# Kernel optimization log

Hardware: AMD Instinct MI355X
Metric: run time of the kernel (lower is better)

## Reference

```python
import jax, jax.numpy as jnp
import numpy as np
from jax import lax

B, S, I, H, O, L = 32, 512, 256, 1024, 256, 3


def setup_inputs() -> dict:
    key = jax.random.key(0)
    ks = jax.random.split(key, 10)
    sc = 0.02
    return {
        "x": jax.random.normal(ks[0], (B, S, I), dtype=jnp.float32),
        "h0": jnp.zeros((B, L, H), dtype=jnp.float32),
        # layer 0 params: gates ordered [z, r, g]
        "Wx0": jax.random.normal(ks[1], (3, H, I), dtype=jnp.float32) * sc,
        "Wh0": jax.random.normal(ks[2], (3, H, H), dtype=jnp.float32) * sc,
        "bh0": jax.random.normal(ks[3], (3, H), dtype=jnp.float32) * sc,
        # layers 1..L-1 params (input dim = H)
        "Wx": jax.random.normal(ks[4], (L - 1, 3, H, H), dtype=jnp.float32) * sc,
        "Wh": jax.random.normal(ks[5], (L - 1, 3, H, H), dtype=jnp.float32) * sc,
        "bh": jax.random.normal(ks[6], (L - 1, 3, H), dtype=jnp.float32) * sc,
        "Wout": jax.random.normal(ks[7], (O, H), dtype=jnp.float32) * sc,
        "bout": jax.random.normal(ks[8], (O,), dtype=jnp.float32) * sc,
    }


def _gru_layer(x_seq, h0, Wx, Wh, bh):
    # x_seq: [S,B,Iin], h0: [B,H], Wx: [3,H,Iin], Wh: [3,H,H], bh: [3,H]
    # Precompute all input projections once (fused GEMM over full sequence).
    xproj = jnp.einsum('sbi,ghi->sbgh', x_seq, Wx)  # [S,B,3,H]

    def step(h, xp):
        z = jax.nn.sigmoid(xp[:, 0] + h @ Wh[0].T + bh[0])
        r = jax.nn.sigmoid(xp[:, 1] + h @ Wh[1].T + bh[1])
        g = jnp.tanh(xp[:, 2] + (r * h) @ Wh[2].T + bh[2])
        h_new = z * h + (1.0 - z) * g
        return h_new, h_new

    h_last, hs = lax.scan(step, h0, xproj)
    return hs, h_last  # hs: [S,B,H]


def reference(x, h0, Wx0, Wh0, bh0, Wx, Wh, bh, Wout, bout):
    seq = jnp.transpose(x, (1, 0, 2))  # [S,B,I]
    cur, hl = _gru_layer(seq, h0[:, 0], Wx0, Wh0, bh0)
    finals = [hl]
    n_extra = Wx.shape[0]
    for i in range(n_extra):  # small fixed layer count
        cur, hl = _gru_layer(cur, h0[:, i + 1], Wx[i], Wh[i], bh[i])
        finals.append(hl)
    out = cur @ Wout.T + bout  # [S,B,O]
    layer_output = jnp.transpose(out, (1, 0, 2))  # [B,S,O]
    hidden_state = jnp.stack(finals, axis=1)  # [B,L,H]
    return layer_output, hidden_state
```

## Files before the change

### kernel.cpp

```cpp
#include <hip/hip_runtime.h>
#include <cstdint>
#include <cstddef>

#define S_  512
#define H_  1024
#define H3  3072
#define OUT_OFF 4194304

typedef __attribute__((ext_vector_type(8))) short  short8;
typedef __attribute__((ext_vector_type(4))) float  f32x4;
typedef __attribute__((ext_vector_type(4))) unsigned short us4;
typedef __attribute__((ext_vector_type(4))) unsigned int   u32x4;
typedef unsigned long long u64;

#define MFMA __builtin_amdgcn_mfma_f32_16x16x32_bf16

static const size_t XP_OFF    = 0;
static const size_t H2_OFF    = 100663296;
static const size_t XBF_OFF   = 134217728;
static const size_t WX0B_OFF  = 142606336;
static const size_t WZR0_OFF  = 144179200;
static const size_t WG0_OFF   = 148373504;
static const size_t WZR1_OFF  = 150470656;
static const size_t WGX1_OFF  = 158859264;
static const size_t WG1_OFF   = 160956416;
static const size_t WZR2_OFF  = 163053568;
static const size_t WGX2_OFF  = 171442176;
static const size_t WG2_OFF   = 173539328;
static const size_t WOUTB_OFF = 175636480;
static const size_t ZBU_OFF   = 176160768;
static const size_t GXB_OFF   = 176553984;
static const size_t HROW_OFF  = 176947200;
static const size_t FLAG_OFF  = 177340416;
static const size_t HH_OFF    = 177344512;
static const size_t RHH_OFF   = 278597632;
static const size_t WS_HIST   = 379654144;
static const size_t WS_BASE   = 177737728;

__device__ inline unsigned short f2bf(float f){
  unsigned u = __builtin_bit_cast(unsigned, f);
  unsigned r = u + 0x7fffu + ((u >> 16) & 1u);
  return (unsigned short)(r >> 16);
}
__device__ inline float bf2f(unsigned short s){
  unsigned u = ((unsigned)s) << 16;
  return __builtin_bit_cast(float, u);
}
__device__ inline unsigned ld_sys(const unsigned* p){
  return __hip_atomic_load(p, __ATOMIC_RELAXED, __HIP_MEMORY_SCOPE_AGENT);
}
__device__ inline void st_sys(unsigned* p, unsigned v){
  __hip_atomic_store(p, v, __ATOMIC_RELAXED, __HIP_MEMORY_SCOPE_AGENT);
}
__device__ inline u64 ld64(const u64* p){
  return __hip_atomic_load(p, __ATOMIC_RELAXED, __HIP_MEMORY_SCOPE_AGENT);
}
__device__ inline void st64(u64* p, u64 v){
  __hip_atomic_store(p, v, __ATOMIC_RELAXED, __HIP_MEMORY_SCOPE_AGENT);
}
template<bool HIST>
__device__ inline u64 LD(const u64* p){
  if constexpr (HIST) return *p; else return ld64(p);
}
__device__ inline short8 mk8u(u64 a, u64 b){
  u32x4 u; u.x = (unsigned)a; u.y = (unsigned)(a >> 32); u.z = (unsigned)b; u.w = (unsigned)(b >> 32);
  return __builtin_bit_cast(short8, u);
}
__device__ inline u64 pk4(float a, float b, float c, float d){
  return (u64)f2bf(a) | ((u64)f2bf(b) << 16) | ((u64)f2bf(c) << 32) | ((u64)f2bf(d) << 48);
}
__device__ inline u64 pk2f(float a, float b){
  return (u64)__builtin_bit_cast(unsigned, a) | ((u64)__builtin_bit_cast(unsigned, b) << 32);
}
__device__ inline float lo32f(u64 u){ return __builtin_bit_cast(float, (unsigned)u); }
__device__ inline float hi32f(u64 u){ return __builtin_bit_cast(float, (unsigned)(u >> 32)); }

__global__ void k_conv(const float* __restrict__ src, unsigned short* __restrict__ dst, int n){
  int i = blockIdx.x*256 + threadIdx.x;
  if (i < n) dst[i] = f2bf(src[i]);
}
__global__ void k_packzr(const float* __restrict__ Wh, const float* __restrict__ Wx,
                         unsigned short* __restrict__ dst){
  size_t i = (size_t)blockIdx.x*256 + threadIdx.x;
  int k = (int)(i & 2047);
  int n = (int)(i >> 11);
  float v = (k < 1024) ? Wh[(size_t)n*1024 + k] : Wx[(size_t)n*1024 + (k - 1024)];
  dst[i] = f2bf(v);
}
__global__ void k_convx(const float* __restrict__ x, unsigned short* __restrict__ xbf){
  int row = blockIdx.x;
  int s = row >> 5, b = row & 31;
  int i = threadIdx.x;
  xbf[(size_t)row*256 + i] = f2bf(x[((size_t)b*S_ + s)*256 + i]);
}

__global__ __launch_bounds__(256) void k_gemm(const unsigned short* __restrict__ A,
                                              const unsigned short* __restrict__ Bw,
                                              const float* __restrict__ bias,
                                              void* __restrict__ Cout,
                                              int Kd, int mode, int Nd){
  __shared__ __align__(16) unsigned short lA[128*40];
  __shared__ __align__(16) unsigned short lB[128*40];
  int bm = blockIdx.y * 128, bn = blockIdx.x * 128;
  int tid = threadIdx.x;
  int w = tid >> 6, lane = tid & 63, q = lane >> 4, cc = lane & 15;
  int wm = (w >> 1) * 64, wn = (w & 1) * 64;
  f32x4 acc[4][4] = {};
  for (int k0 = 0; k0 < Kd; k0 += 32){
    #pragma unroll
    for (int i = 0; i < 2; i++){
      int idx = tid + i*256;
      int r = idx >> 2, ch = idx & 3;
      int m = bm + r;
      int arow = (mode == 0) ? m : ((m & 511)*32 + (m >> 9));
      *(u32x4*)(lA + r*40 + ch*8) = *(const u32x4*)(A + (size_t)arow*Kd + k0 + ch*8);
      *(u32x4*)(lB + r*40 + ch*8) = *(const u32x4*)(Bw + (size_t)(bn + r)*Kd + k0 + ch*8);
    }
    __syncthreads();
    short8 af[4], bfv[4];
    #pragma unroll
    for (int i = 0; i < 4; i++) af[i]  = *(const short8*)(lA + (wm + i*16 + cc)*40 + q*8);
    #pragma unroll
    for (int i = 0; i < 4; i++) bfv[i] = *(const short8*)(lB + (wn + i*16 + cc)*40 + q*8);
    #pragma unroll
    for (int i = 0; i < 4; i++)
      #pragma unroll
      for (int j = 0; j < 4; j++)
        acc[i][j] = MFMA(af[i], bfv[j], acc[i][j], 0, 0, 0);
    __syncthreads();
  }
  if (mode == 0){
    unsigned short* xp = (unsigned short*)Cout;
    #pragma unroll
    for (int i = 0; i < 4; i++){
      #pragma unroll
      for (int j = 0; j < 4; j++){
        int m = bm + wm + i*16 + q*4;
        int n = bn + wn + j*16 + cc;
        float bv = bias[n];
        int s = m >> 5, b0 = m & 31;
        us4 pk;
        #pragma unroll
        for (int reg = 0; reg < 4; reg++) pk[reg] = f2bf(acc[i][j][reg] + bv);
        *(us4*)(xp + ((size_t)s*H3 + n)*32 + b0) = pk;
      }
    }
  } else {
    float* C = (float*)Cout;
    #pragma unroll
    for (int i = 0; i < 4; i++){
      #pragma unroll
      for (int j = 0; j < 4; j++){
        int m = bm + wm + i*16 + q*4;
        int n = bn + wn + j*16 + cc;
        float bv = bias[n];
        #pragma unroll
        for (int reg = 0; reg < 4; reg++)
          C[(size_t)(m + reg)*Nd + n] = acc[i][j][reg] + bv;
      }
    }
  }
}

__device__ inline void gbar(unsigned* flags, unsigned ep){
  __syncthreads();
  if (threadIdx.x == 0) st_sys(flags + blockIdx.x, ep);
  if (threadIdx.x < 64){
    for (;;){
      unsigned v0 = ld_sys(flags + threadIdx.x);
      unsigned v1 = ld_sys(flags + 64 + threadIdx.x);
      unsigned v2 = ld_sys(flags + 128 + threadIdx.x);
      unsigned v3 = ld_sys(flags + 192 + threadIdx.x);
      if (__all((v0 >= ep) && (v1 >= ep) && (v2 >= ep) && (v3 >= ep))) break;
      __builtin_amdgcn_s_sleep(1);
    }
  }
  __syncthreads();
}

template<int NITER, bool HIST>
__device__ inline void matvec(const u64* p0, const unsigned short* wp,
                              f32x4& acc0, f32x4& acc1){
  u64 buf[2][4][4];
  #pragma unroll
  for (int ii = 0; ii < 4; ii++){
    const u64* p = p0 + ii*256;
    buf[0][ii][0] = LD<HIST>(p);      buf[0][ii][1] = LD<HIST>(p + 32);
    buf[0][ii][2] = LD<HIST>(p + 16); buf[0][ii][3] = LD<HIST>(p + 48);
  }
  constexpr int NCH = NITER / 4;
  #pragma unroll
  for (int ch = 0; ch < NCH; ch++){
    const int cur = ch & 1, nxt = cur ^ 1;
    if (ch + 1 < NCH){
      #pragma unroll
      for (int ii = 0; ii < 4; ii++){
        const u64* p = p0 + ((ch+1)*4 + ii)*256;
        buf[nxt][ii][0] = LD<HIST>(p);      buf[nxt][ii][1] = LD<HIST>(p + 32);
        buf[nxt][ii][2] = LD<HIST>(p + 16); buf[nxt][ii][3] = LD<HIST>(p + 48);
      }
    }
    #pragma unroll
    for (int ii = 0; ii < 4; ii++){
      short8 bw = *(const short8*)(wp + (ch*4 + ii)*32);
      acc0 = MFMA(mk8u(buf[cur][ii][0], buf[cur][ii][1]), bw, acc0, 0, 0, 0);
      acc1 = MFMA(mk8u(buf[cur][ii][2], buf[cur][ii][3]), bw, acc1, 0, 0, 0);
    }
  }
}

template<int MODE>
__global__ __launch_bounds__(256, 1) void k_fused(char* __restrict__ ws,
                                                  const float* __restrict__ h0,
                                                  const float* __restrict__ bh,
                                                  float* __restrict__ outp,
                                                  u64* __restrict__ hh,
                                                  u64* __restrict__ rhh){
  constexpr bool HIST = (MODE >= 1);
  constexpr bool DF   = (MODE == 2);

  __shared__ __align__(16) unsigned short wlds[65920];
  __shared__ __align__(16) float red[2][3][64][10];
  __shared__ float rtA[16*33];
  __shared__ float rtB[16*33];

  const int tid = threadIdx.x;
  const int w = tid >> 6, lane = tid & 63, q = (lane >> 4) & 3, c = lane & 15;
  const int i = blockIdx.x;

  const int lz   = 1 + (i >> 7);
  const int g2   = (i >> 6) & 1;
  const int n2   = (i & 63) << 4;
  const bool isl0 = (i < 128);
  const int g1   = (i >> 6) & 1;
  const int lgx  = 1 + ((i >> 6) & 1);
  const int n1   = (i & 63) << 4;
  const bool hasB = (i < 192);
  const int lb   = i >> 6;
  const int nb   = (i & 63) << 4;

  const unsigned short* xp = (const unsigned short*)(ws + XP_OFF);
  u64* h2u   = (u64*)(ws + H2_OFF);
  u64* zbu   = (u64*)(ws + ZBU_OFF);
  u64* gxb   = (u64*)(ws + GXB_OFF);
  float* hrow = (float*)(ws + HROW_OFF);
  unsigned* flags = (unsigned*)(ws + FLAG_OFF);
  unsigned* flagA = flags + 256;
  unsigned* flagB = flags + 512;

  int catA = (lane < 32) ? 0 : ((lane < 48) ? 1 : 2);
  int idxA = 0;
  if (lane < 32)      idxA = 64*((w < 2) ? lz : (lz-1)) + (w & 1)*32 + lane;
  else if (lane < 48) idxA = 64*(isl0 ? 0 : (lgx-1)) + w*16 + (lane - 32);
  else if (lane == 48){
    if (w == 0){ idxA = 64*lz + (i & 63); catA = 0; }
    else if (w == 1){ idxA = (isl0 ? 0 : 64*lgx) + (i & 63); catA = 1; }
  }
  const unsigned* pollA = flagB + idxA;
  int catB = 1; int idxB = 0;
  if (lane < 16){ idxB = ((lb == 2) ? 192 : 64) + w*16 + lane; catB = 0; }
  else if (w == 0 && lane == 16){ idxB = ((lb == 2) ? 128 : 0) + (i & 63); catB = 0; }
  else if (w == 0 && lane == 17 && lb >= 1){ idxB = ((lb == 1) ? 128 : 192) + (i & 63); catB = 0; }
  const unsigned* pollB = flagA + idxB;

  {
    const unsigned short* src2 = (const unsigned short*)(ws + (lz == 1 ? WZR1_OFF : WZR2_OFF))
                                 + (size_t)(g2*1024 + n2)*2048;
    for (int idx = tid; idx < 4096; idx += 256){
      int kc = idx & 255, row = idx >> 8;
      u32x4 v = *(const u32x4*)(src2 + (size_t)row*2048 + kc*8);
      *(u32x4*)(wlds + row*2056 + kc*8) = v;
    }
    const unsigned short* src1 = isl0
      ? (const unsigned short*)(ws + WZR0_OFF) + (size_t)(g1*1024 + n1)*1024
      : (const unsigned short*)(ws + (lgx == 1 ? WGX1_OFF : WGX2_OFF)) + (size_t)n1*1024;
    for (int idx = tid; idx < 2048; idx += 256){
      int kc = idx & 127, row = idx >> 7;
      u32x4 v = *(const u32x4*)(src1 + (size_t)row*1024 + kc*8);
      *(u32x4*)(wlds + 32896 + row*1032 + kc*8) = v;
    }
    if (hasB){
      const unsigned short* srcb = (const unsigned short*)(ws + (lb == 0 ? WG0_OFF : (lb == 1 ? WG1_OFF : WG2_OFF)))
                                   + (size_t)nb*1024;
      for (int idx = tid; idx < 2048; idx += 256){
        int kc = idx & 127, row = idx >> 7;
        u32x4 v = *(const u32x4*)(srcb + (size_t)row*1024 + kc*8);
        *(u32x4*)(wlds + 49408 + row*1032 + kc*8) = v;
      }
    }
  }
  const float biasT2 = bh[(size_t)(lz-1)*H3 + g2*1024 + n2 + c];
  const float biasGX = isl0 ? 0.f : bh[(size_t)(lgx-1)*H3 + 2048 + n1 + c];

  if (hasB){
    for (int idx = tid; idx < 512; idx += 256){
      int n = idx >> 5, b = idx & 31;
      float v = h0[((size_t)b*3 + lb)*H_ + nb + n];
      hrow[((size_t)lb*1024 + nb + n)*32 + b] = v;
      rtA[n*33 + b] = v;
    }
  }
  __syncthreads();
  if (hasB && tid < 128){
    int b = tid & 31, p2 = tid >> 5;
    u64 pkv = pk4(rtA[(4*p2+0)*33+b], rtA[(4*p2+1)*33+b], rtA[(4*p2+2)*33+b], rtA[(4*p2+3)*33+b]);
    st64(hh + (size_t)(HIST ? lb : 0)*24576 + (size_t)lb*8192 + (size_t)((nb >> 2) + p2)*32 + b, pkv);
  }
  unsigned ep = 1;
  if constexpr (DF){
    __syncthreads();
    if (tid == 0 && hasB) st_sys(flagB + i, (unsigned)(lb + 1));
  } else {
    gbar(flags, ep); ep++;
  }

  for (int T = 0; T < 514; T++){
    const int t2 = T - lz;
    const bool actT2 = (unsigned)t2 < 512u;
    const int t1 = isl0 ? T : (T - lgx);
    const bool actT1 = (unsigned)t1 < 512u;
    const int tb = T - lb;
    const bool actB = hasB && ((unsigned)tb < 512u);

    const u64* hslotR = hh + (size_t)(HIST ? T : 0)*24576;
    u64*       rslot  = rhh + (size_t)(HIST ? T : 0)*24576;

    if constexpr (DF){
      const bool req = (catA == 0) ? actT2 : ((catA == 1) ? actT1 : false);
      const unsigned epw = (unsigned)(T + 1);
      for (;;){
        unsigned v = req ? ld_sys(pollA) : 0xFFFFFFFFu;
        if (__all(v >= epw)) break;
        __builtin_amdgcn_s_sleep(2);
      }
    }

    u64 hpreA[8]; us4 xpreA[2]; u64 hpreL0[8];
    if (actT2 && w == 0 && g2 == 1){
      const u64* hb = hslotR + (size_t)lz*8192 + (size_t)((n2 + c) >> 2)*32 + q*4;
      #pragma unroll
      for (int mt = 0; mt < 2; mt++)
        #pragma unroll
        for (int r = 0; r < 4; r++) hpreA[mt*4+r] = LD<HIST>(hb + mt*16 + r);
    }
    if (actT1 && w == 1 && isl0){
      const unsigned short* xr = xp + ((size_t)t1*H3 + g1*1024 + n1 + c)*32 + q*4;
      xpreA[0] = *(const us4*)(xr);
      xpreA[1] = *(const us4*)(xr + 16);
      if (g1 == 1){
        const u64* hb = hslotR + (size_t)((n1 + c) >> 2)*32 + q*4;
        #pragma unroll
        for (int mt = 0; mt < 2; mt++)
          #pragma unroll
          for (int r = 0; r < 4; r++) hpreL0[mt*4+r] = LD<HIST>(hb + mt*16 + r);
      }
    }

    f32x4 z20 = {0,0,0,0}, z21 = {0,0,0,0};
    f32x4 z10 = {0,0,0,0}, z11 = {0,0,0,0};
    if (actT2){
      const u64* p0 = hslotR + (size_t)((w < 2) ? lz : (lz-1))*8192 + (size_t)((w & 1)*128 + q*2)*32 + c;
      const unsigned short* wp = wlds + c*2056 + w*512 + q*8;
      matvec<16, HIST>(p0, wp, z20, z21);
    }
    if (actT1){
      const u64* p0 = hslotR + (size_t)(isl0 ? 0 : (lgx-1))*8192 + (size_t)(w*64 + q*2)*32 + c;
      const unsigned short* wp = wlds + 32896 + c*1032 + w*256 + q*8;
      matvec<8, HIST>(p0, wp, z10, z11);
    }
    if (actT2 && w > 0){
      float* p = &red[0][w-1][lane][0];
      #pragma unroll
      for (int r = 0; r < 4; r++){ p[r] = z20[r]; p[4+r] = z21[r]; }
    }
    if (actT1 && w != 1){
      float* p = &red[1][(w == 0) ? 0 : (w-1)][lane][0];
      #pragma unroll
      for (int r = 0; r < 4; r++){ p[r] = z10[r]; p[4+r] = z11[r]; }
    }
    __syncthreads();
    if (w == 0 && actT2){
      #pragma unroll
      for (int s = 0; s < 3; s++){
        const float* p = &red[0][s][lane][0];
        #pragma unroll
        for (int r = 0; r < 4; r++){ z20[r] += p[r]; z21[r] += p[4+r]; }
      }
      const int sh = (c & 3)*16;
      #pragma unroll
      for (int mt = 0; mt < 2; mt++){
        float f[4];
        #pragma unroll
        for (int r = 0; r < 4; r++){
          float pre = (mt ? z21[r] : z20[r]) + biasT2;
          f[r] = 1.0f / (1.0f + __expf(-pre));
        }
        if (g2 == 0){
          u64* zp = zbu + ((size_t)lz*1024 + n2 + c)*16 + mt*8 + q*2;
          st64(zp, pk2f(f[0], f[1])); st64(zp + 1, pk2f(f[2], f[3]));
        } else {
          #pragma unroll
          for (int r = 0; r < 4; r++){
            int b = mt*16 + q*4 + r;
            rtA[c*33 + b] = f[r] * bf2f((unsigned short)(hpreA[mt*4+r] >> sh));
          }
        }
      }
    }
    if (w == 1 && actT1){
      #pragma unroll
      for (int s = 0; s < 3; s++){
        const float* p = &red[1][s][lane][0];
        #pragma unroll
        for (int r = 0; r < 4; r++){ z10[r] += p[r]; z11[r] += p[4+r]; }
      }
      if (isl0){
        const int sh = (c & 3)*16;
        #pragma unroll
        for (int mt = 0; mt < 2; mt++){
          us4 xv = xpreA[mt];
          float f[4];
          #pragma unroll
          for (int r = 0; r < 4; r++){
            float pre = (mt ? z11[r] : z10[r]) + bf2f(xv[r]);
            f[r] = 1.0f / (1.0f + __expf(-pre));
          }
          if (g1 == 0){
            u64* zp = zbu + ((size_t)n1 + c)*16 + mt*8 + q*2;
            st64(zp, pk2f(f[0], f[1])); st64(zp + 1, pk2f(f[2], f[3]));
          } else {
            #pragma unroll
            for (int r = 0; r < 4; r++){
              int b = mt*16 + q*4 + r;
              rtB[c*33 + b] = f[r] * bf2f((unsigned short)(hpreL0[mt*4+r] >> sh));
            }
          }
        }
      } else {
        #pragma unroll
        for (int mt = 0; mt < 2; mt++){
          float f[4];
          #pragma unroll
          for (int r = 0; r < 4; r++) f[r] = (mt ? z11[r] : z10[r]) + biasGX;
          u64* gp = gxb + ((size_t)lgx*1024 + n1 + c)*16 + mt*8 + q*2;
          st64(gp, pk2f(f[0], f[1])); st64(gp + 1, pk2f(f[2], f[3]));
        }
      }
    }
    __syncthreads();
    if (g2 == 1 && actT2 && tid < 128){
      int b = tid & 31, p2 = tid >> 5;
      st64(rslot + (size_t)lz*8192 + (size_t)((n2 >> 2) + p2)*32 + b,
           pk4(rtA[(4*p2+0)*33+b], rtA[(4*p2+1)*33+b], rtA[(4*p2+2)*33+b], rtA[(4*p2+3)*33+b]));
    }
    if (isl0 && g1 == 1 && actT1 && tid >= 128){
      int tt = tid - 128; int b = tt & 31, p2 = tt >> 5;
      st64(rslot + (size_t)((n1 >> 2) + p2)*32 + b,
           pk4(rtB[(4*p2+0)*33+b], rtB[(4*p2+1)*33+b], rtB[(4*p2+2)*33+b], rtB[(4*p2+3)*33+b]));
    }
    if constexpr (DF){
      __syncthreads();
      if (tid == 0 && (actT2 || actT1)) st_sys(flagA + i, (unsigned)(T + 1));
      {
        const bool req = (catB == 0) && actB;
        const unsigned epw = (unsigned)(T + 1);
        for (;;){
          unsigned v = req ? ld_sys(pollB) : 0xFFFFFFFFu;
          if (__all(v >= epw)) break;
          __builtin_amdgcn_s_sleep(2);
        }
      }
    } else {
      gbar(flags, ep); ep++;
    }

    u64 zpreB[4], gpreB[4]; us4 xpreB[2]; f32x4 hpre4[2];
    if (actB && w == 0){
      const u64* zp = zbu + ((size_t)lb*1024 + nb + c)*16 + q*2;
      zpreB[0] = ld64(zp);     zpreB[1] = ld64(zp + 1);
      zpreB[2] = ld64(zp + 8); zpreB[3] = ld64(zp + 9);
      if (lb == 0){
        const unsigned short* xr = xp + ((size_t)tb*H3 + 2048 + nb + c)*32 + q*4;
        xpreB[0] = *(const us4*)(xr);
        xpreB[1] = *(const us4*)(xr + 16);
      } else {
        const u64* gp = gxb + ((size_t)lb*1024 + nb + c)*16 + q*2;
        gpreB[0] = ld64(gp);     gpreB[1] = ld64(gp + 1);
        gpreB[2] = ld64(gp + 8); gpreB[3] = ld64(gp + 9);
      }
      const float* hp0 = hrow + ((size_t)lb*1024 + nb + c)*32 + q*4;
      hpre4[0] = *(const f32x4*)(hp0);
      hpre4[1] = *(const f32x4*)(hp0 + 16);
    }

    f32x4 gb0 = {0,0,0,0}, gb1 = {0,0,0,0};
    if (actB){
      const u64* p0 = (const u64*)rslot + (size_t)lb*8192 + (size_t)(w*64 + q*2)*32 + c;
      const unsigned short* wp = wlds + 49408 + c*1032 + w*256 + q*8;
      matvec<8, HIST>(p0, wp, gb0, gb1);
      if (w > 0){
        float* p = &red[0][w-1][lane][0];
        #pragma unroll
        for (int r = 0; r < 4; r++){ p[r] = gb0[r]; p[4+r] = gb1[r]; }
      }
    }
    __syncthreads();
    if (actB && w == 0){
      #pragma unroll
      for (int s = 0; s < 3; s++){
        const float* p = &red[0][s][lane][0];
        #pragma unroll
        for (int r = 0; r < 4; r++){ gb0[r] += p[r]; gb1[r] += p[4+r]; }
      }
      #pragma unroll
      for (int mt = 0; mt < 2; mt++){
        float gadd[4];
        if (lb == 0){
          us4 xv = xpreB[mt];
          #pragma unroll
          for (int r = 0; r < 4; r++) gadd[r] = bf2f(xv[r]);
        } else {
          gadd[0] = lo32f(gpreB[mt*2]);   gadd[1] = hi32f(gpreB[mt*2]);
          gadd[2] = lo32f(gpreB[mt*2+1]); gadd[3] = hi32f(gpreB[mt*2+1]);
        }
        float zf[4] = { lo32f(zpreB[mt*2]),   hi32f(zpreB[mt*2]),
                        lo32f(zpreB[mt*2+1]), hi32f(zpreB[mt*2+1]) };
        f32x4 h4 = hpre4[mt];
        f32x4 hn4;
        #pragma unroll
        for (int r = 0; r < 4; r++){
          float gpre = (mt ? gb1[r] : gb0[r]) + gadd[r];
          float gv = tanhf(gpre);
          float hnv = zf[r]*h4[r] + (1.0f - zf[r])*gv;
          hn4[r] = hnv;
          rtA[c*33 + mt*16 + q*4 + r] = hnv;
          if (tb == 511) outp[OUT_OFF + ((size_t)(mt*16 + q*4 + r)*3 + lb)*H_ + nb + c] = hnv;
        }
        *(f32x4*)(hrow + ((size_t)lb*1024 + nb + c)*32 + mt*16 + q*4) = hn4;
      }
    }
    __syncthreads();
    if (actB && tid < 128){
      int b = tid & 31, p2 = tid >> 5;
      u64 pkv = pk4(rtA[(4*p2+0)*33+b], rtA[(4*p2+1)*33+b], rtA[(4*p2+2)*33+b], rtA[(4*p2+3)*33+b]);
      st64(hh + (size_t)(HIST ? (T + 1) : 0)*24576 + (size_t)lb*8192 + (size_t)((nb >> 2) + p2)*32 + b, pkv);
      if (lb == 2) *(u64*)(h2u + ((size_t)tb*32 + b)*256 + (nb >> 2) + p2) = pkv;
    }
    if constexpr (DF){
      __syncthreads();
      if (tid == 0 && actB) st_sys(flagB + i, (unsigned)(T + 2));
    } else {
      gbar(flags, ep); ep++;
    }
  }
  (void)ep;
}

extern "C" void kernel_launch(void* const* d_in, const int* in_sizes, int n_in,
                              void* d_out, int out_size, void* d_ws, size_t ws_size,
                              hipStream_t stream){
  (void)in_sizes; (void)n_in; (void)out_size;
  if (ws_size < WS_BASE) return;
  const bool hist = (ws_size >= WS_HIST);

  const float* x    = (const float*)d_in[0];
  const float* h0   = (const float*)d_in[1];
  const float* Wx0  = (const float*)d_in[2];
  const float* Wh0  = (const float*)d_in[3];
  const float* bh0  = (const float*)d_in[4];
  const float* Wx   = (const float*)d_in[5];
  const float* Wh   = (const float*)d_in[6];
  const float* bh   = (const float*)d_in[7];
  const float* Wout = (const float*)d_in[8];
  const float* bout = (const float*)d_in[9];
  float* out = (float*)d_out;

  char* ws = (char*)d_ws;
  unsigned short* xp    = (unsigned short*)(ws + XP_OFF);
  unsigned short* h2    = (unsigned short*)(ws + H2_OFF);
  unsigned short* xbf   = (unsigned short*)(ws + XBF_OFF);
  unsigned short* wx0b  = (unsigned short*)(ws + WX0B_OFF);
  unsigned short* wzr0  = (unsigned short*)(ws + WZR0_OFF);
  unsigned short* wg0   = (unsigned short*)(ws + WG0_OFF);
  unsigned short* wzr1  = (unsigned short*)(ws + WZR1_OFF);
  unsigned short* wgx1  = (unsigned short*)(ws + WGX1_OFF);
  unsigned short* wg1   = (unsigned short*)(ws + WG1_OFF);
  unsigned short* wzr2  = (unsigned short*)(ws + WZR2_OFF);
  unsigned short* wgx2  = (unsigned short*)(ws + WGX2_OFF);
  unsigned short* wg2   = (unsigned short*)(ws + WG2_OFF);
  unsigned short* woutb = (unsigned short*)(ws + WOUTB_OFF);
  u64* hh  = (u64*)(ws + HH_OFF);
  u64* rhh = hist ? (u64*)(ws + RHH_OFF) : (hh + 24576);

  hipMemsetAsync(ws + FLAG_OFF, 0, 4096, stream);

  k_conv<<<3072, 256, 0, stream>>>(Wx0, wx0b, 786432);
  k_conv<<<8192, 256, 0, stream>>>(Wh0, wzr0, 2097152);
  k_conv<<<4096, 256, 0, stream>>>(Wh0 + 2097152, wg0, 1048576);
  k_packzr<<<16384, 256, 0, stream>>>(Wh, Wx, wzr1);
  k_conv<<<4096, 256, 0, stream>>>(Wx + 2097152, wgx1, 1048576);
  k_conv<<<4096, 256, 0, stream>>>(Wh + 2097152, wg1, 1048576);
  k_packzr<<<16384, 256, 0, stream>>>(Wh + 3145728, Wx + 3145728, wzr2);
  k_conv<<<4096, 256, 0, stream>>>(Wx + 5242880, wgx2, 1048576);
  k_conv<<<4096, 256, 0, stream>>>(Wh + 5242880, wg2, 1048576);
  k_conv<<<1024, 256, 0, stream>>>(Wout, woutb, 262144);
  k_convx<<<16384, 256, 0, stream>>>(x, xbf);

  {
    dim3 g(24, 128);
    k_gemm<<<g, 256, 0, stream>>>(xbf, wx0b, bh0, (void*)xp, 256, 0, H3);
  }
  if (hist) k_fused<2><<<256, 256, 0, stream>>>(ws, h0, bh, out, hh, rhh);
  else      k_fused<0><<<256, 256, 0, stream>>>(ws, h0, bh, out, hh, rhh);
  {
    dim3 g(2, 128);
    k_gemm<<<g, 256, 0, stream>>>(h2, woutb, bout, (void*)out, 1024, 1, 256);
  }
}
```

Before: 7.225 ms.

## Split phase-A completion flags per producer wave with release stores, drop sleeps

Replaces the single per-block phase-A flag with separate flags per producer role (z/r gate, layer-0 gate, r*h publish), each set by the specific wave that produced the data using release-ordered atomic stores. Consumers poll only the flags they depend on, and some block-wide barriers before flag publication are removed. The r*h and h packing stores are moved to a single wave so that wave can release its flag right after its own stores. Spin-wait sleeps are removed to cut wake-up latency. The finer-grained dependencies should shorten the serial per-timestep critical path, at the cost of more flag traffic and busier polling. Correctness now depends on each release store covering exactly the data its consumers read.

Result: no change. 7.189 ms (-0.5%).

```diff
diff --git a/kernel.cpp b/kernel.cpp
--- a/kernel.cpp
+++ b/kernel.cpp
@@ -52,6 +52,9 @@
 __device__ inline void st_sys(unsigned* p, unsigned v){
   __hip_atomic_store(p, v, __ATOMIC_RELAXED, __HIP_MEMORY_SCOPE_AGENT);
 }
+__device__ inline void st_rel(unsigned* p, unsigned v){
+  __hip_atomic_store(p, v, __ATOMIC_RELEASE, __HIP_MEMORY_SCOPE_AGENT);
+}
 __device__ inline u64 ld64(const u64* p){
   return __hip_atomic_load(p, __ATOMIC_RELAXED, __HIP_MEMORY_SCOPE_AGENT);
 }
@@ -245,8 +248,10 @@
   u64* gxb   = (u64*)(ws + GXB_OFF);
   float* hrow = (float*)(ws + HROW_OFF);
   unsigned* flags = (unsigned*)(ws + FLAG_OFF);
-  unsigned* flagA = flags + 256;
-  unsigned* flagB = flags + 512;
+  unsigned* fA2 = flags;
+  unsigned* fA0 = flags + 256;
+  unsigned* fA1 = flags + 512;
+  unsigned* fB0 = flags + 768;
 
   int catA = (lane < 32) ? 0 : ((lane < 48) ? 1 : 2);
   int idxA = 0;
@@ -256,12 +261,24 @@
     if (w == 0){ idxA = 64*lz + (i & 63); catA = 0; }
     else if (w == 1){ idxA = (isl0 ? 0 : 64*lgx) + (i & 63); catA = 1; }
   }
-  const unsigned* pollA = flagB + idxA;
-  int catB = 1; int idxB = 0;
-  if (lane < 16){ idxB = ((lb == 2) ? 192 : 64) + w*16 + lane; catB = 0; }
-  else if (w == 0 && lane == 16){ idxB = ((lb == 2) ? 128 : 0) + (i & 63); catB = 0; }
-  else if (w == 0 && lane == 17 && lb >= 1){ idxB = ((lb == 1) ? 128 : 192) + (i & 63); catB = 0; }
-  const unsigned* pollB = flagA + idxB;
+  const unsigned* pollA = fB0 + idxA;
+  const unsigned* pollB = fA0;
+  bool reqB_lane = false;
+  if (hasB){
+    if (lane < 16){
+      pollB = (lb == 0) ? (fA2 + 16*w + lane)
+                        : (fA0 + ((lb == 1) ? 64 : 192) + 16*w + lane);
+      reqB_lane = true;
+    } else if (w == 0 && lane == 16){
+      pollB = (lb == 0) ? (fA1 + (i & 63))
+            : (lb == 1) ? (fA0 + (i & 63))
+                        : (fA0 + 128 + (i & 63));
+      reqB_lane = true;
+    } else if (w == 0 && lane == 17 && lb >= 1){
+      pollB = (lb == 1) ? (fA1 + 128 + (i & 63)) : (fA1 + 192 + (i & 63));
+      reqB_lane = true;
+    }
+  }
 
   {
     const unsigned short* src2 = (const unsigned short*)(ws + (lz == 1 ? WZR1_OFF : WZR2_OFF))
@@ -301,15 +318,19 @@
     }
   }
   __syncthreads();
-  if (hasB && tid < 128){
-    int b = tid & 31, p2 = tid >> 5;
-    u64 pkv = pk4(rtA[(4*p2+0)*33+b], rtA[(4*p2+1)*33+b], rtA[(4*p2+2)*33+b], rtA[(4*p2+3)*33+b]);
-    st64(hh + (size_t)(HIST ? lb : 0)*24576 + (size_t)lb*8192 + (size_t)((nb >> 2) + p2)*32 + b, pkv);
+  if (hasB && tid < 64){
+    int b = tid & 31, p2b = (tid >> 5)*2;
+    #pragma unroll
+    for (int pp = 0; pp < 2; pp++){
+      int p2 = p2b + pp;
+      u64 pkv = pk4(rtA[(4*p2+0)*33+b], rtA[(4*p2+1)*33+b], rtA[(4*p2+2)*33+b], rtA[(4*p2+3)*33+b]);
+      st64(hh + (size_t)(HIST ? lb : 0)*24576 + (size_t)lb*8192 + (size_t)((nb >> 2) + p2)*32 + b, pkv);
+    }
   }
   unsigned ep = 1;
   if constexpr (DF){
+    if (tid == 0 && hasB) st_rel(fB0 + i, (unsigned)(lb + 1));
     __syncthreads();
-    if (tid == 0 && hasB) st_sys(flagB + i, (unsigned)(lb + 1));
   } else {
     gbar(flags, ep); ep++;
   }
@@ -331,7 +352,6 @@
       for (;;){
         unsigned v = req ? ld_sys(pollA) : 0xFFFFFFFFu;
         if (__all(v >= epw)) break;
-        __builtin_amdgcn_s_sleep(2);
       }
     }
 
@@ -405,6 +425,9 @@
             rtA[c*33 + b] = f[r] * bf2f((unsigned short)(hpreA[mt*4+r] >> sh));
           }
         }
+      }
+      if constexpr (DF){
+        if (g2 == 0 && lane == 0) st_rel(fA0 + i, (unsigned)(T + 1));
       }
     }
     if (w == 1 && actT1){
@@ -436,6 +459,9 @@
             }
           }
         }
+        if constexpr (DF){
+          if (g1 == 0 && lane == 0) st_rel(fA1 + i, (unsigned)(T + 1));
+        }
       } else {
         #pragma unroll
         for (int mt = 0; mt < 2; mt++){
@@ -445,30 +471,42 @@
           u64* gp = gxb + ((size_t)lgx*1024 + n1 + c)*16 + mt*8 + q*2;
           st64(gp, pk2f(f[0], f[1])); st64(gp + 1, pk2f(f[2], f[3]));
         }
+        if constexpr (DF){
+          if (lane == 0) st_rel(fA1 + i, (unsigned)(T + 1));
+        }
       }
     }
     __syncthreads();
-    if (g2 == 1 && actT2 && tid < 128){
-      int b = tid & 31, p2 = tid >> 5;
-      st64(rslot + (size_t)lz*8192 + (size_t)((n2 >> 2) + p2)*32 + b,
-           pk4(rtA[(4*p2+0)*33+b], rtA[(4*p2+1)*33+b], rtA[(4*p2+2)*33+b], rtA[(4*p2+3)*33+b]));
-    }
-    if (isl0 && g1 == 1 && actT1 && tid >= 128){
-      int tt = tid - 128; int b = tt & 31, p2 = tt >> 5;
-      st64(rslot + (size_t)((n1 >> 2) + p2)*32 + b,
-           pk4(rtB[(4*p2+0)*33+b], rtB[(4*p2+1)*33+b], rtB[(4*p2+2)*33+b], rtB[(4*p2+3)*33+b]));
+    if (g2 == 1 && actT2 && tid < 64){
+      int b = tid & 31, p2b = (tid >> 5)*2;
+      #pragma unroll
+      for (int pp = 0; pp < 2; pp++){
+        int p2 = p2b + pp;
+        st64(rslot + (size_t)lz*8192 + (size_t)((n2 >> 2) + p2)*32 + b,
+             pk4(rtA[(4*p2+0)*33+b], rtA[(4*p2+1)*33+b], rtA[(4*p2+2)*33+b], rtA[(4*p2+3)*33+b]));
+      }
+      if constexpr (DF){
+        if (tid == 0) st_rel(fA0 + i, (unsigned)(T + 1));
+      }
+    }
+    if (isl0 && g1 == 1 && actT1 && tid >= 128 && tid < 192){
+      int tt = tid - 128; int b = tt & 31, p2b = (tt >> 5)*2;
+      #pragma unroll
+      for (int pp = 0; pp < 2; pp++){
+        int p2 = p2b + pp;
+        st64(rslot + (size_t)((n1 >> 2) + p2)*32 + b,
+             pk4(rtB[(4*p2+0)*33+b], rtB[(4*p2+1)*33+b], rtB[(4*p2+2)*33+b], rtB[(4*p2+3)*33+b]));
+      }
+      if constexpr (DF){
+        if (tid == 128) st_rel(fA2 + (i - 64), (unsigned)(T + 1));
+      }
     }
     if constexpr (DF){
-      __syncthreads();
-      if (tid == 0 && (actT2 || actT1)) st_sys(flagA + i, (unsigned)(T + 1));
-      {
-        const bool req = (catB == 0) && actB;
-        const unsigned epw = (unsigned)(T + 1);
-        for (;;){
-          unsigned v = req ? ld_sys(pollB) : 0xFFFFFFFFu;
-          if (__all(v >= epw)) break;
-          __builtin_amdgcn_s_sleep(2);
-        }
+      const unsigned epw = (unsigned)(T + 1);
+      const bool req = reqB_lane && actB;
+      for (;;){
+        unsigned v = req ? ld_sys(pollB) : 0xFFFFFFFFu;
+        if (__all(v >= epw)) break;
       }
     } else {
       gbar(flags, ep); ep++;
@@ -539,16 +577,19 @@
         *(f32x4*)(hrow + ((size_t)lb*1024 + nb + c)*32 + mt*16 + q*4) = hn4;
       }
     }
-    __syncthreads();
-    if (actB && tid < 128){
-      int b = tid & 31, p2 = tid >> 5;
-      u64 pkv = pk4(rtA[(4*p2+0)*33+b], rtA[(4*p2+1)*33+b], rtA[(4*p2+2)*33+b], rtA[(4*p2+3)*33+b]);
-      st64(hh + (size_t)(HIST ? (T + 1) : 0)*24576 + (size_t)lb*8192 + (size_t)((nb >> 2) + p2)*32 + b, pkv);
-      if (lb == 2) *(u64*)(h2u + ((size_t)tb*32 + b)*256 + (nb >> 2) + p2) = pkv;
+    if (actB && tid < 64){
+      int b = tid & 31, p2b = (tid >> 5)*2;
+      #pragma unroll
+      for (int pp = 0; pp < 2; pp++){
+        int p2 = p2b + pp;
+        u64 pkv = pk4(rtA[(4*p2+0)*33+b], rtA[(4*p2+1)*33+b], rtA[(4*p2+2)*33+b], rtA[(4*p2+3)*33+b]);
+        st64(hh + (size_t)(HIST ? (T + 1) : 0)*24576 + (size_t)lb*8192 + (size_t)((nb >> 2) + p2)*32 + b, pkv);
+        if (lb == 2) *(u64*)(h2u + ((size_t)tb*32 + b)*256 + (nb >> 2) + p2) = pkv;
+      }
     }
     if constexpr (DF){
+      if (actB && tid == 0) st_rel(fB0 + i, (unsigned)(T + 2));
       __syncthreads();
-      if (tid == 0 && actB) st_sys(flagB + i, (unsigned)(T + 2));
     } else {
       gbar(flags, ep); ep++;
     }
```
